# Kernel tuning notes

Measured on AMD Instinct MI355X. Metric: run time of the kernel, lower is better.

## Reference

```python
import jax, jax.numpy as jnp
import numpy as np

WINDOW = (2, 8, 8)
DIM = 180
HEADS = 6
NW = 64  # number of distinct window masks


def _get_position_index(ws):
    d, h, w = ws
    coords = np.stack(np.meshgrid(np.arange(d), np.arange(h), np.arange(w), indexing='ij'))  # [3,d,h,w]
    cf = coords.reshape(3, -1)
    rel = cf[:, :, None] - cf[:, None, :]  # [3,N,N]
    rel = rel.transpose(1, 2, 0).astype(np.int64)
    rel[:, :, 0] += d - 1
    rel[:, :, 1] += h - 1
    rel[:, :, 2] += w - 1
    rel[:, :, 0] *= (2 * h - 1) * (2 * w - 1)
    rel[:, :, 1] *= 2 * w - 1
    return rel.sum(-1)  # [N,N]


def _get_sine_position_encoding(HW, num_pos_feats, temperature=10000.0, normalize=True):
    scale = 2 * np.pi
    not_mask = np.ones((1, HW[0], HW[1]), dtype=np.float32)
    y_embed = not_mask.cumsum(1)
    x_embed = not_mask.cumsum(2)
    if normalize:
        eps = 1e-6
        y_embed = y_embed / (y_embed[:, -1:, :] + eps) * scale
        x_embed = x_embed / (x_embed[:, :, -1:] + eps) * scale
    dim_t = np.arange(num_pos_feats, dtype=np.float32)
    dim_t = temperature ** (2 * (dim_t // 2) / num_pos_feats)
    pos_x = x_embed[:, :, :, None] / dim_t
    pos_y = y_embed[:, :, :, None] / dim_t
    pos_x = np.stack((np.sin(pos_x[:, :, :, 0::2]), np.cos(pos_x[:, :, :, 1::2])), axis=4).reshape(1, HW[0], HW[1], -1)
    pos_y = np.stack((np.sin(pos_y[:, :, :, 0::2]), np.cos(pos_y[:, :, :, 1::2])), axis=4).reshape(1, HW[0], HW[1], -1)
    pos = np.concatenate((pos_y, pos_x), axis=3)  # [1,H,W,2*npf]
    return pos.reshape(1, HW[0] * HW[1], -1)  # [1, H*W, dim]


REL_IDX = _get_position_index(WINDOW)                      # [128,128] int
POS_BIAS = _get_sine_position_encoding(WINDOW[1:], DIM // 2)  # [1,64,180]


def setup_inputs() -> dict:
    key = jax.random.key(0)
    ks = jax.random.split(key, 8)
    B_, N, C = 1024, 128, DIM
    x = jax.random.normal(ks[0], (B_, N, C), dtype=jnp.float32)
    # 0 / -1e4 additive window mask (shifted-window style), nW windows
    m = jax.random.uniform(ks[1], (NW, N, N))
    mask = jnp.where(m < 0.9, 0.0, -1e4).astype(jnp.float32)
    rpb_table = jax.random.normal(ks[2], (675, HEADS), dtype=jnp.float32) * 0.02
    W_qkv_self = jax.random.normal(ks[3], (3 * C, C), dtype=jnp.float32) * (C ** -0.5)
    W_qkv_mut = jax.random.normal(ks[4], (3 * C, C), dtype=jnp.float32) * (C ** -0.5)
    W_proj = jax.random.normal(ks[5], (C, 2 * C), dtype=jnp.float32) * ((2 * C) ** -0.5)
    b_proj = jax.random.normal(ks[6], (C,), dtype=jnp.float32) * 0.01
    return {"x": x, "mask": mask, "rpb_table": rpb_table, "W_qkv_self": W_qkv_self,
            "W_qkv_mut": W_qkv_mut, "W_proj": W_proj, "b_proj": b_proj}


def _qkv(x, W, H):
    B_, N, C = x.shape
    hd = C // H
    y = jnp.einsum('bnc,oc->bno', x, W)  # torch Linear: x @ W.T
    y = y.reshape(B_, N, 3, H, hd).transpose(2, 0, 3, 1, 4)  # [3,B_,H,N,hd]
    return y[0], y[1], y[2]


def _attention(q, k, v, mask, bias, scale):
    # q,k,v: [B_,H,N,hd]; mask: [nW,>=N,>=N] or None; bias: [H,N,N] or None
    B_, H, N, hd = q.shape
    attn = jnp.einsum('bhnd,bhmd->bhnm', q * scale, k)
    if bias is not None:
        attn = attn + bias[None]
    if mask is not None:
        nW = mask.shape[0]
        attn = attn.reshape(B_ // nW, nW, H, N, N) + mask[None, :, None, :N, :N]
        attn = attn.reshape(B_, H, N, N)
    attn = jax.nn.softmax(attn, axis=-1)
    out = jnp.einsum('bhnm,bhmd->bhnd', attn, v)
    return out.transpose(0, 2, 1, 3).reshape(B_, N, H * hd)


def reference(x, mask, rpb_table, W_qkv_self, W_qkv_mut, W_proj, b_proj):
    B_, N, C = x.shape
    H = HEADS
    hd = C // H
    scale = hd ** -0.5
    rel_idx = jnp.asarray(REL_IDX)
    pos_bias = jnp.asarray(POS_BIAS, dtype=x.dtype)

    # self attention with relative position bias
    q, k, v = _qkv(x, W_qkv_self, H)
    bias = rpb_table[rel_idx[:N, :N].reshape(-1)].reshape(N, N, H).transpose(2, 0, 1)  # [H,N,N]
    x_self = _attention(q, k, v, mask, bias, scale)

    # mutual attention between the two temporal halves
    pb = jnp.tile(pos_bias, (1, 2, 1))  # [1,N,C]
    qm, km, vm = _qkv(x + pb, W_qkv_mut, H)
    half = N // 2
    q1, q2 = qm[:, :, :half], qm[:, :, half:]
    k1, k2 = km[:, :, :half], km[:, :, half:]
    v1, v2 = vm[:, :, :half], vm[:, :, half:]
    x1 = _attention(q2, k1, v1, mask, None, scale)
    x2 = _attention(q1, k2, v2, mask, None, scale)
    x_out = jnp.concatenate([jnp.concatenate([x1, x2], axis=1), x_self], axis=2)  # [B_,N,2C]

    return jnp.einsum('bnc,oc->bno', x_out, W_proj) + b_proj
```

## Files before the change

### kernel.cpp

```cpp
#include <hip/hip_runtime.h>
#include <hip/hip_bf16.h>


typedef unsigned short u16;
typedef unsigned int   u32;

#define NTOK 128
#define CDIM 180
#define NHEAD 6
#define XSTR 188
#define KVSTR 36
#define KVSZ  4640
#define QSTR 36
#define SLSTR 33
#define QKSCALE 0.18257418583505536f

__device__ __forceinline__ float bflo(u32 u){ return __uint_as_float(u << 16); }
__device__ __forceinline__ float bfhi(u32 u){ return __uint_as_float(u & 0xFFFF0000u); }
__device__ __forceinline__ float bf2f(u16 v){ return __uint_as_float(((u32)v) << 16); }

__device__ __forceinline__ int kvrow(int r){ return r * KVSTR + ((r >> 4) << 2); }

template<bool F32> __device__ __forceinline__ float ld1(const void* p, size_t i) {
  if constexpr (F32) return reinterpret_cast<const float*>(p)[i];
  else               return bf2f(reinterpret_cast<const u16*>(p)[i]);
}
template<bool F32> __device__ __forceinline__ float2 ld2(const void* p, size_t i) {
  if constexpr (F32) return *reinterpret_cast<const float2*>(reinterpret_cast<const float*>(p) + i);
  else {
    u32 r = *reinterpret_cast<const u32*>(reinterpret_cast<const u16*>(p) + i);
    return float2{bflo(r), bfhi(r)};
  }
}
template<bool F32> __device__ __forceinline__ float4 ld4(const void* p, size_t i) {
  if constexpr (F32) return *reinterpret_cast<const float4*>(reinterpret_cast<const float*>(p) + i);
  else {
    uint2 r = *reinterpret_cast<const uint2*>(reinterpret_cast<const u16*>(p) + i);
    return float4{bflo(r.x), bfhi(r.x), bflo(r.y), bfhi(r.y)};
  }
}

__global__ void detect_dtype(const u32* __restrict__ xw, int* __restrict__ flag) {
  __shared__ int cnt[256];
  int c = 0;
  for (int i = threadIdx.x; i < 4096; i += 256) {
    u32 e = (xw[i] >> 7) & 0xFF;
    c += (e >= 0x58 && e <= 0x90) ? 1 : 0;
  }
  cnt[threadIdx.x] = c;
  __syncthreads();
  if (threadIdx.x == 0) {
    int t = 0;
    for (int i = 0; i < 256; ++i) t += cnt[i];
    flag[0] = (t >= 2458) ? 1 : 0;
  }
}

template<bool F32>
__device__ void body(const void* __restrict__ x,
                     const void* __restrict__ mask,
                     const void* __restrict__ rpb,
                     const void* __restrict__ Wqs,
                     const void* __restrict__ Wqm,
                     const void* __restrict__ Wp,
                     const void* __restrict__ bp,
                     float* __restrict__ out,
                     float* x_s, float* k_s, float* v_s, float* sq_s)
{
  const int tid = threadIdx.x;
  const int b   = blockIdx.x;
  const int n   = tid >> 2;
  const int j   = tid & 3;
  const int w64 = b & 63;

  const int nt  = tid & 31;
  const int ot  = tid >> 5;
  const bool act = (ot < 15);
  const int grp = ot / 5;
  const int lr0 = (ot - grp * 5) * 6;

  const int rp = tid & 127;
  const int og = __builtin_amdgcn_readfirstlane(tid >> 7);
  float acc[45];
  #pragma unroll
  for (int o2 = 0; o2 < 45; ++o2) acc[o2] = 0.f;

  const int bi_d = n >> 6, bi_h = (n >> 3) & 7, bi_w = n & 7;

  {
    const size_t xbase = (size_t)b * (NTOK * CDIM);
    for (int i = tid * 4; i < NTOK * CDIM; i += 2048) {
      float4 f = ld4<F32>(x, xbase + i);
      int r = i / CDIM, c = i - r * CDIM;
      float* dst = &x_s[r * XSTR + c];
      dst[0] = f.x; dst[1] = f.y; dst[2] = f.z; dst[3] = f.w;
    }
  }
  if (tid < NTOK) {
    const int kb = kvrow(tid);
    k_s[kb + 30] = 0.f; k_s[kb + 31] = 0.f;
    v_s[kb + 30] = 0.f; v_s[kb + 31] = 0.f;
  }

  for (int pass = 0; pass < 2; ++pass) {
    const bool self = (pass == 0);
    const void* W = self ? Wqs : Wqm;
    if (!self) {
      __syncthreads();
      for (int i = tid; i < NTOK * CDIM; i += 512) {
        int r = i / CDIM, c = i - r * CDIM;
        int n64 = r & 63;
        int t = (c < 90) ? c : (c - 90);
        float e = (c < 90) ? (float)((n64 >> 3) + 1) : (float)((n64 & 7) + 1);
        float embed = e * 0.78539807f;
        float expo  = (float)(t & ~1) * (1.0f / 90.0f);
        float arg   = embed * exp2f(-13.2877124f * expo);
        float pbv   = (t & 1) ? cosf(arg) : sinf(arg);
        x_s[r * XSTR + c] += pbv;
      }
    }
    for (int h = 0; h < NHEAD; ++h) {
      __syncthreads();
      if (act) {
        float a[4][6];
        #pragma unroll
        for (int i = 0; i < 4; ++i)
          #pragma unroll
          for (int rr = 0; rr < 6; ++rr) a[i][rr] = 0.f;
        const size_t wb = (size_t)(grp * 180 + h * 30 + lr0) * CDIM;
        const float* xr = &x_s[nt * XSTR];
        #pragma unroll 3
        for (int c = 0; c < CDIM; c += 4) {
          float4 wv[6];
          #pragma unroll
          for (int rr = 0; rr < 6; ++rr)
            wv[rr] = ld4<F32>(W, wb + (size_t)rr * CDIM + c);
          #pragma unroll
          for (int i = 0; i < 4; ++i) {
            float4 xv = *reinterpret_cast<const float4*>(xr + i * (32 * XSTR) + c);
            #pragma unroll
            for (int rr = 0; rr < 6; ++rr)
              a[i][rr] = fmaf(xv.x, wv[rr].x,
                         fmaf(xv.y, wv[rr].y,
                         fmaf(xv.z, wv[rr].z,
                         fmaf(xv.w, wv[rr].w, a[i][rr]))));
          }
        }
        #pragma unroll
        for (int i = 0; i < 4; ++i) {
          const int n2 = 32 * i + nt;
          #pragma unroll
          for (int rr = 0; rr < 6; ++rr) {
            const int lr = lr0 + rr;
            const float val = a[i][rr];
            if (grp == 0)      sq_s[n2 * QSTR + lr] = val * QKSCALE;
            else if (grp == 1) k_s[kvrow(n2) + lr] = val;
            else               v_s[kvrow(n2) + lr] = val;
          }
        }
      }
      __syncthreads();
      float qfull[32];
      {
        const float* qr = &sq_s[n * QSTR];
        #pragma unroll
        for (int kk = 0; kk < 7; ++kk) {
          float4 t4 = *reinterpret_cast<const float4*>(qr + 4 * kk);
          qfull[4*kk]   = t4.x; qfull[4*kk+1] = t4.y;
          qfull[4*kk+2] = t4.z; qfull[4*kk+3] = t4.w;
        }
        float2 t2 = *reinterpret_cast<const float2*>(qr + 28);
        qfull[28] = t2.x; qfull[29] = t2.y;
        qfull[30] = 0.f;  qfull[31] = 0.f;
      }
      __syncthreads();
      float o[32];
      #pragma unroll
      for (int d = 0; d < 32; ++d) o[d] = 0.f;
      float m = -1e30f, l = 0.f;

      int jbeg, jcount, kbase;
      if (self) { jbeg = j * 32; jcount = 32; kbase = 0; }
      else      { jbeg = j * 16; jcount = 16; kbase = (n < 64) ? 64 : 0; }
      const int il = self ? n : (n & 63);
      const size_t mbase = (size_t)w64 * (NTOK * NTOK) + (size_t)il * NTOK;

      for (int jj = 0; jj < jcount; jj += 4) {
        const int jl = jbeg + jj;
        const int jg = kbase + jl;
        const float* kb = &k_s[kvrow(jg)];
        float s[4];
        #pragma unroll
        for (int u = 0; u < 4; ++u) {
          const float* kr = kb + u * KVSTR;
          float t0 = 0.f, t1 = 0.f, t2 = 0.f, t3 = 0.f;
          #pragma unroll
          for (int kk = 0; kk < 8; ++kk) {
            float4 kv = *reinterpret_cast<const float4*>(kr + 4 * kk);
            t0 = fmaf(qfull[4 * kk],     kv.x, t0);
            t1 = fmaf(qfull[4 * kk + 1], kv.y, t1);
            t2 = fmaf(qfull[4 * kk + 2], kv.z, t2);
            t3 = fmaf(qfull[4 * kk + 3], kv.w, t3);
          }
          float sv = (t0 + t1) + (t2 + t3);
          sv += ld1<F32>(mask, mbase + (size_t)(jl + u));
          if (self) {
            const int jv = jl + u;
            const int dj = jv >> 6, hj = (jv >> 3) & 7, wj = jv & 7;
            const int idx = (bi_d - dj + 1) * 225 + (bi_h - hj + 7) * 15 + (bi_w - wj + 7);
            sv += ld1<F32>(rpb, (size_t)idx * 6 + h);
          }
          s[u] = sv;
        }
        float M = fmaxf(fmaxf(fmaxf(s[0], s[1]), fmaxf(s[2], s[3])), m);
        float corr = __expf(m - M);
        float p0 = __expf(s[0] - M), p1 = __expf(s[1] - M);
        float p2 = __expf(s[2] - M), p3 = __expf(s[3] - M);
        l = l * corr + ((p0 + p1) + (p2 + p3));
        const float* v0 = &v_s[kvrow(jg)];
        const float* v1 = v0 + KVSTR;
        const float* v2 = v1 + KVSTR;
        const float* v3 = v2 + KVSTR;
        #pragma unroll
        for (int kk = 0; kk < 8; ++kk) {
          float4 a0 = *reinterpret_cast<const float4*>(v0 + 4 * kk);
          float4 a1 = *reinterpret_cast<const float4*>(v1 + 4 * kk);
          float4 a2 = *reinterpret_cast<const float4*>(v2 + 4 * kk);
          float4 a3 = *reinterpret_cast<const float4*>(v3 + 4 * kk);
          o[4*kk]   = fmaf(o[4*kk],   corr, fmaf(p0, a0.x, fmaf(p1, a1.x, fmaf(p2, a2.x, p3 * a3.x))));
          o[4*kk+1] = fmaf(o[4*kk+1], corr, fmaf(p0, a0.y, fmaf(p1, a1.y, fmaf(p2, a2.y, p3 * a3.y))));
          o[4*kk+2] = fmaf(o[4*kk+2], corr, fmaf(p0, a0.z, fmaf(p1, a1.z, fmaf(p2, a2.z, p3 * a3.z))));
          o[4*kk+3] = fmaf(o[4*kk+3], corr, fmaf(p0, a0.w, fmaf(p1, a1.w, fmaf(p2, a2.w, p3 * a3.w))));
        }
        m = M;
      }
      {
        #pragma unroll
        for (int s2 = 1; s2 <= 2; s2 <<= 1) {
          float m2 = __shfl_xor(m, s2);
          float l2 = __shfl_xor(l, s2);
          float M  = fmaxf(m, m2);
          float e1 = __expf(m - M);
          float e2 = __expf(m2 - M);
          l = l * e1 + l2 * e2;
          #pragma unroll
          for (int d = 0; d < 30; ++d) {
            float o2v = __shfl_xor(o[d], s2);
            o[d] = o[d] * e1 + o2v * e2;
          }
          m = M;
        }
        if (j == 0) {
          const int r = self ? n : ((n + 64) & 127);
          float* srow = &sq_s[r * SLSTR];
          const float inv = 1.0f / l;
          #pragma unroll
          for (int d = 0; d < 30; ++d) srow[d] = o[d] * inv;
        }
      }
      __syncthreads();
      {
        const int cb = self ? (CDIM + h * 30) : (h * 30);
        float s0[30];
        #pragma unroll
        for (int d = 0; d < 30; ++d) s0[d] = sq_s[rp * SLSTR + d];
        const size_t wrow = (size_t)(og * 45) * 360 + cb;
        #pragma unroll
        for (int o2 = 0; o2 < 45; ++o2) {
          const size_t wr = wrow + (size_t)o2 * 360;
          float t0 = 0.f;
          #pragma unroll
          for (int d = 0; d < 30; d += 2) {
            float2 w2 = ld2<F32>(Wp, wr + d);
            t0 = fmaf(s0[d], w2.x, fmaf(s0[d + 1], w2.y, t0));
          }
          acc[o2] += t0;
        }
      }
    }
  }

  {
    float* o0 = out + ((size_t)b * NTOK + rp) * CDIM + og * 45;
    #pragma unroll
    for (int o2 = 0; o2 < 45; ++o2) {
      float bb = ld1<F32>(bp, og * 45 + o2);
      o0[o2] = acc[o2] + bb;
    }
  }
}

__global__ __launch_bounds__(512) void fused_all(
    const void* __restrict__ x,    const void* __restrict__ mask,
    const void* __restrict__ rpb,  const void* __restrict__ Wqs,
    const void* __restrict__ Wqm,  const void* __restrict__ Wp,
    const void* __restrict__ bp,   const int* __restrict__ flag,
    float* __restrict__ out)
{
  __shared__ __align__(16) float x_s[NTOK * XSTR];
  __shared__ __align__(16) float k_s[KVSZ];
  __shared__ __align__(16) float v_s[KVSZ];
  __shared__ __align__(16) float sq_s[NTOK * QSTR];
  if (flag[0]) body<false>(x, mask, rpb, Wqs, Wqm, Wp, bp, out, x_s, k_s, v_s, sq_s);
  else         body<true >(x, mask, rpb, Wqs, Wqm, Wp, bp, out, x_s, k_s, v_s, sq_s);
}

extern "C" void kernel_launch(void* const* d_in, const int* in_sizes, int n_in,
                              void* d_out, int out_size, void* d_ws, size_t ws_size,
                              hipStream_t stream) {
  int* flag = (int*)d_ws;
  detect_dtype<<<1, 256, 0, stream>>>((const u32*)d_in[0], flag);
  fused_all<<<1024, 512, 0, stream>>>(d_in[0], d_in[1], d_in[2], d_in[3],
                                      d_in[4], d_in[5], d_in[6], flag,
                                      (float*)d_out);
}
```

Measured before the change: 2.461 ms.

## Process two query rows per thread with 8-way key split in attention

Each thread now handles two adjacent query rows, and the key range for a row is split across 8 lanes instead of 4. Every K and V vector read from shared memory is reused for both rows, halving LDS traffic per FMA. The cost is doubled accumulator and q registers (o0/o1, qf0/qf1), which risks spills or lower occupancy given the existing 45-float acc array, plus an extra shuffle-reduction stage.

```diff
diff --git a/kernel.cpp b/kernel.cpp
--- a/kernel.cpp
+++ b/kernel.cpp
@@ -69,9 +69,11 @@
 {
   const int tid = threadIdx.x;
   const int b   = blockIdx.x;
-  const int n   = tid >> 2;
-  const int j   = tid & 3;
   const int w64 = b & 63;
+
+  const int g  = tid >> 3;
+  const int j8 = tid & 7;
+  const int n0 = g * 2, n1 = n0 + 1;
 
   const int nt  = tid & 31;
   const int ot  = tid >> 5;
@@ -85,7 +87,8 @@
   #pragma unroll
   for (int o2 = 0; o2 < 45; ++o2) acc[o2] = 0.f;
 
-  const int bi_d = n >> 6, bi_h = (n >> 3) & 7, bi_w = n & 7;
+  const int b0d = n0 >> 6, b0h = (n0 >> 3) & 7, b0w = n0 & 7;
+  const int b1d = n1 >> 6, b1h = (n1 >> 3) & 7, b1w = n1 & 7;
 
   {
     const size_t xbase = (size_t)b * (NTOK * CDIM);
@@ -160,63 +163,80 @@
         }
       }
       __syncthreads();
-      float qfull[32];
+      float qf0[32], qf1[32];
       {
-        const float* qr = &sq_s[n * QSTR];
+        const float* qr0 = &sq_s[n0 * QSTR];
+        const float* qr1 = &sq_s[n1 * QSTR];
         #pragma unroll
         for (int kk = 0; kk < 7; ++kk) {
-          float4 t4 = *reinterpret_cast<const float4*>(qr + 4 * kk);
-          qfull[4*kk]   = t4.x; qfull[4*kk+1] = t4.y;
-          qfull[4*kk+2] = t4.z; qfull[4*kk+3] = t4.w;
-        }
-        float2 t2 = *reinterpret_cast<const float2*>(qr + 28);
-        qfull[28] = t2.x; qfull[29] = t2.y;
-        qfull[30] = 0.f;  qfull[31] = 0.f;
-      }
-      __syncthreads();
-      float o[32];
+          float4 t4 = *reinterpret_cast<const float4*>(qr0 + 4 * kk);
+          qf0[4*kk] = t4.x; qf0[4*kk+1] = t4.y; qf0[4*kk+2] = t4.z; qf0[4*kk+3] = t4.w;
+          float4 u4 = *reinterpret_cast<const float4*>(qr1 + 4 * kk);
+          qf1[4*kk] = u4.x; qf1[4*kk+1] = u4.y; qf1[4*kk+2] = u4.z; qf1[4*kk+3] = u4.w;
+        }
+        float2 t2 = *reinterpret_cast<const float2*>(qr0 + 28);
+        qf0[28] = t2.x; qf0[29] = t2.y; qf0[30] = 0.f; qf0[31] = 0.f;
+        float2 u2 = *reinterpret_cast<const float2*>(qr1 + 28);
+        qf1[28] = u2.x; qf1[29] = u2.y; qf1[30] = 0.f; qf1[31] = 0.f;
+      }
+      __syncthreads();
+      float o0[32], o1[32];
       #pragma unroll
-      for (int d = 0; d < 32; ++d) o[d] = 0.f;
-      float m = -1e30f, l = 0.f;
+      for (int d = 0; d < 32; ++d) { o0[d] = 0.f; o1[d] = 0.f; }
+      float m0 = -1e30f, l0 = 0.f, m1 = -1e30f, l1 = 0.f;
 
       int jbeg, jcount, kbase;
-      if (self) { jbeg = j * 32; jcount = 32; kbase = 0; }
-      else      { jbeg = j * 16; jcount = 16; kbase = (n < 64) ? 64 : 0; }
-      const int il = self ? n : (n & 63);
-      const size_t mbase = (size_t)w64 * (NTOK * NTOK) + (size_t)il * NTOK;
+      if (self) { jbeg = j8 * 16; jcount = 16; kbase = 0; }
+      else      { jbeg = j8 * 8;  jcount = 8;  kbase = (n0 < 64) ? 64 : 0; }
+      const int il0 = self ? n0 : (n0 & 63);
+      const size_t mbase0 = (size_t)w64 * (NTOK * NTOK) + (size_t)il0 * NTOK;
+      const size_t mbase1 = mbase0 + NTOK;
 
       for (int jj = 0; jj < jcount; jj += 4) {
         const int jl = jbeg + jj;
         const int jg = kbase + jl;
         const float* kb = &k_s[kvrow(jg)];
-        float s[4];
+        float s0[4], s1[4];
         #pragma unroll
         for (int u = 0; u < 4; ++u) {
           const float* kr = kb + u * KVSTR;
-          float t0 = 0.f, t1 = 0.f, t2 = 0.f, t3 = 0.f;
+          float a0 = 0.f, a1 = 0.f, a2 = 0.f, a3 = 0.f;
+          float c0 = 0.f, c1 = 0.f, c2 = 0.f, c3 = 0.f;
           #pragma unroll
           for (int kk = 0; kk < 8; ++kk) {
             float4 kv = *reinterpret_cast<const float4*>(kr + 4 * kk);
-            t0 = fmaf(qfull[4 * kk],     kv.x, t0);
-            t1 = fmaf(qfull[4 * kk + 1], kv.y, t1);
-            t2 = fmaf(qfull[4 * kk + 2], kv.z, t2);
-            t3 = fmaf(qfull[4 * kk + 3], kv.w, t3);
-          }
-          float sv = (t0 + t1) + (t2 + t3);
-          sv += ld1<F32>(mask, mbase + (size_t)(jl + u));
+            a0 = fmaf(qf0[4*kk],   kv.x, a0);
+            a1 = fmaf(qf0[4*kk+1], kv.y, a1);
+            a2 = fmaf(qf0[4*kk+2], kv.z, a2);
+            a3 = fmaf(qf0[4*kk+3], kv.w, a3);
+            c0 = fmaf(qf1[4*kk],   kv.x, c0);
+            c1 = fmaf(qf1[4*kk+1], kv.y, c1);
+            c2 = fmaf(qf1[4*kk+2], kv.z, c2);
+            c3 = fmaf(qf1[4*kk+3], kv.w, c3);
+          }
+          float sv0 = (a0 + a1) + (a2 + a3);
+          float sv1 = (c0 + c1) + (c2 + c3);
+          sv0 += ld1<F32>(mask, mbase0 + (size_t)(jl + u));
+          sv1 += ld1<F32>(mask, mbase1 + (size_t)(jl + u));
           if (self) {
             const int jv = jl + u;
             const int dj = jv >> 6, hj = (jv >> 3) & 7, wj = jv & 7;
-            const int idx = (bi_d - dj + 1) * 225 + (bi_h - hj + 7) * 15 + (bi_w - wj + 7);
-            sv += ld1<F32>(rpb, (size_t)idx * 6 + h);
-          }
-          s[u] = sv;
-        }
-        float M = fmaxf(fmaxf(fmaxf(s[0], s[1]), fmaxf(s[2], s[3])), m);
-        float corr = __expf(m - M);
-        float p0 = __expf(s[0] - M), p1 = __expf(s[1] - M);
-        float p2 = __expf(s[2] - M), p3 = __expf(s[3] - M);
-        l = l * corr + ((p0 + p1) + (p2 + p3));
+            const int i0 = (b0d - dj + 1) * 225 + (b0h - hj + 7) * 15 + (b0w - wj + 7);
+            const int i1 = (b1d - dj + 1) * 225 + (b1h - hj + 7) * 15 + (b1w - wj + 7);
+            sv0 += ld1<F32>(rpb, (size_t)i0 * 6 + h);
+            sv1 += ld1<F32>(rpb, (size_t)i1 * 6 + h);
+          }
+          s0[u] = sv0; s1[u] = sv1;
+        }
+        float M0 = fmaxf(fmaxf(fmaxf(s0[0], s0[1]), fmaxf(s0[2], s0[3])), m0);
+        float M1 = fmaxf(fmaxf(fmaxf(s1[0], s1[1]), fmaxf(s1[2], s1[3])), m1);
+        float cr0 = __expf(m0 - M0), cr1 = __expf(m1 - M1);
+        float p00 = __expf(s0[0] - M0), p01 = __expf(s0[1] - M0);
+        float p02 = __expf(s0[2] - M0), p03 = __expf(s0[3] - M0);
+        float p10 = __expf(s1[0] - M1), p11 = __expf(s1[1] - M1);
+        float p12 = __expf(s1[2] - M1), p13 = __expf(s1[3] - M1);
+        l0 = l0 * cr0 + ((p00 + p01) + (p02 + p03));
+        l1 = l1 * cr1 + ((p10 + p11) + (p12 + p13));
         const float* v0 = &v_s[kvrow(jg)];
         const float* v1 = v0 + KVSTR;
         const float* v2 = v1 + KVSTR;
@@ -227,43 +247,65 @@
           float4 a1 = *reinterpret_cast<const float4*>(v1 + 4 * kk);
           float4 a2 = *reinterpret_cast<const float4*>(v2 + 4 * kk);
           float4 a3 = *reinterpret_cast<const float4*>(v3 + 4 * kk);
-          o[4*kk]   = fmaf(o[4*kk],   corr, fmaf(p0, a0.x, fmaf(p1, a1.x, fmaf(p2, a2.x, p3 * a3.x))));
-          o[4*kk+1] = fmaf(o[4*kk+1], corr, fmaf(p0, a0.y, fmaf(p1, a1.y, fmaf(p2, a2.y, p3 * a3.y))));
-          o[4*kk+2] = fmaf(o[4*kk+2], corr, fmaf(p0, a0.z, fmaf(p1, a1.z, fmaf(p2, a2.z, p3 * a3.z))));
-          o[4*kk+3] = fmaf(o[4*kk+3], corr, fmaf(p0, a0.w, fmaf(p1, a1.w, fmaf(p2, a2.w, p3 * a3.w))));
-        }
-        m = M;
+          o0[4*kk]   = fmaf(o0[4*kk],   cr0, fmaf(p00, a0.x, fmaf(p01, a1.x, fmaf(p02, a2.x, p03 * a3.x))));
+          o0[4*kk+1] = fmaf(o0[4*kk+1], cr0, fmaf(p00, a0.y, fmaf(p01, a1.y, fmaf(p02, a2.y, p03 * a3.y))));
+          o0[4*kk+2] = fmaf(o0[4*kk+2], cr0, fmaf(p00, a0.z, fmaf(p01, a1.z, fmaf(p02, a2.z, p03 * a3.z))));
+          o0[4*kk+3] = fmaf(o0[4*kk+3], cr0, fmaf(p00, a0.w, fmaf(p01, a1.w, fmaf(p02, a2.w, p03 * a3.w))));
+          o1[4*kk]   = fmaf(o1[4*kk],   cr1, fmaf(p10, a0.x, fmaf(p11, a1.x, fmaf(p12, a2.x, p13 * a3.x))));
+          o1[4*kk+1] = fmaf(o1[4*kk+1], cr1, fmaf(p10, a0.y, fmaf(p11, a1.y, fmaf(p12, a2.y, p13 * a3.y))));
+          o1[4*kk+2] = fmaf(o1[4*kk+2], cr1, fmaf(p10, a0.z, fmaf(p11, a1.z, fmaf(p12, a2.z, p13 * a3.z))));
+          o1[4*kk+3] = fmaf(o1[4*kk+3], cr1, fmaf(p10, a0.w, fmaf(p11, a1.w, fmaf(p12, a2.w, p13 * a3.w))));
+        }
+        m0 = M0; m1 = M1;
       }
       {
         #pragma unroll
-        for (int s2 = 1; s2 <= 2; s2 <<= 1) {
-          float m2 = __shfl_xor(m, s2);
-          float l2 = __shfl_xor(l, s2);
-          float M  = fmaxf(m, m2);
-          float e1 = __expf(m - M);
-          float e2 = __expf(m2 - M);
-          l = l * e1 + l2 * e2;
+        for (int s2 = 1; s2 <= 4; s2 <<= 1) {
+          float mm = __shfl_xor(m0, s2);
+          float ll = __shfl_xor(l0, s2);
+          float M  = fmaxf(m0, mm);
+          float e1 = __expf(m0 - M);
+          float e2 = __expf(mm - M);
+          l0 = l0 * e1 + ll * e2;
           #pragma unroll
           for (int d = 0; d < 30; ++d) {
-            float o2v = __shfl_xor(o[d], s2);
-            o[d] = o[d] * e1 + o2v * e2;
-          }
-          m = M;
-        }
-        if (j == 0) {
-          const int r = self ? n : ((n + 64) & 127);
+            float ov = __shfl_xor(o0[d], s2);
+            o0[d] = o0[d] * e1 + ov * e2;
+          }
+          m0 = M;
+          float mn = __shfl_xor(m1, s2);
+          float ln = __shfl_xor(l1, s2);
+          float N  = fmaxf(m1, mn);
+          float f1 = __expf(m1 - N);
+          float f2 = __expf(mn - N);
+          l1 = l1 * f1 + ln * f2;
+          #pragma unroll
+          for (int d = 0; d < 30; ++d) {
+            float ov = __shfl_xor(o1[d], s2);
+            o1[d] = o1[d] * f1 + ov * f2;
+          }
+          m1 = N;
+        }
+        if (j8 == 0) {
+          const int r = self ? n0 : ((n0 + 64) & 127);
           float* srow = &sq_s[r * SLSTR];
-          const float inv = 1.0f / l;
-          #pragma unroll
-          for (int d = 0; d < 30; ++d) srow[d] = o[d] * inv;
+          const float inv = 1.0f / l0;
+          #pragma unroll
+          for (int d = 0; d < 30; ++d) srow[d] = o0[d] * inv;
+        } else if (j8 == 4) {
+          const int r = self ? n1 : ((n1 + 64) & 127);
+          float* srow = &sq_s[r * SLSTR];
+          const float inv = 1.0f / l1;
+          #pragma unroll
+          for (int d = 0; d < 30; ++d) srow[d] = o1[d] * inv;
         }
       }
       __syncthreads();
       {
         const int cb = self ? (CDIM + h * 30) : (h * 30);
-        float s0[30];
-        #pragma unroll
-        for (int d = 0; d < 30; ++d) s0[d] = sq_s[rp * SLSTR + d];
+        float s0p[30];
+        #pragma unroll
+        for (int d = 0; d < 30; ++d) s0p[d] = sq_s[rp * SLSTR + d];
         const size_t wrow = (size_t)(og * 45) * 360 + cb;
         #pragma unroll
         for (int o2 = 0; o2 < 45; ++o2) {
@@ -272,7 +314,7 @@
           #pragma unroll
           for (int d = 0; d < 30; d += 2) {
             float2 w2 = ld2<F32>(Wp, wr + d);
-            t0 = fmaf(s0[d], w2.x, fmaf(s0[d + 1], w2.y, t0));
+            t0 = fmaf(s0p[d], w2.x, fmaf(s0p[d + 1], w2.y, t0));
           }
           acc[o2] += t0;
         }
```

Measured after the change: 2.411 ms. 2.0% less time.

## Compute QKV projections with split-bf16 MFMA and pre-converted weights

Applied to the files above, without the earlier changes.

Replaces the scalar FP32 FMA QKV projection with bf16 MFMA 16x16x32 instructions. FP32 precision is emulated by splitting x and the weights into hi/lo bf16 parts and issuing three MFMAs. A separate kernel converts both QKV weight matrices into padded hi/lo bf16 buffers in the workspace. Activations are stored in shared memory as hi/lo bf16, and the positional encoding is applied by recombining, adding, and re-splitting. The old FP32 path is kept as a fallback when the workspace is too small. The change trades an extra conversion kernel and some precision risk from dropping the lo*lo term for much higher matrix throughput in the projection stage.

```diff
diff --git a/kernel.cpp b/kernel.cpp
--- a/kernel.cpp
+++ b/kernel.cpp
@@ -8,16 +8,33 @@
 #define NTOK 128
 #define CDIM 180
 #define NHEAD 6
-#define XSTR 188
 #define KVSTR 36
 #define KVSZ  4640
 #define QSTR 36
 #define SLSTR 33
+#define XH   200
+#define WROWS 1081
+#define WCOL 192
+#define XSTR 188
 #define QKSCALE 0.18257418583505536f
+
+typedef __attribute__((ext_vector_type(8))) short bf16x8v;
+typedef __attribute__((ext_vector_type(4))) float f32x4v;
 
 __device__ __forceinline__ float bflo(u32 u){ return __uint_as_float(u << 16); }
 __device__ __forceinline__ float bfhi(u32 u){ return __uint_as_float(u & 0xFFFF0000u); }
 __device__ __forceinline__ float bf2f(u16 v){ return __uint_as_float(((u32)v) << 16); }
+
+__device__ __forceinline__ u16 f2bf(float f){
+  u32 u = __float_as_uint(f);
+  u32 r = u + 0x7FFFu + ((u >> 16) & 1u);
+  return (u16)(r >> 16);
+}
+__device__ __forceinline__ void split2(float f, u16& h, u16& l){
+  h = f2bf(f);
+  float rem = f - bf2f(h);
+  l = f2bf(rem);
+}
 
 __device__ __forceinline__ int kvrow(int r){ return r * KVSTR + ((r >> 4) << 2); }
 
@@ -38,6 +55,15 @@
     uint2 r = *reinterpret_cast<const uint2*>(reinterpret_cast<const u16*>(p) + i);
     return float4{bflo(r.x), bfhi(r.x), bflo(r.y), bfhi(r.y)};
   }
+}
+
+__device__ __forceinline__ float posenc(int c, int n64) {
+  int t = (c < 90) ? c : (c - 90);
+  float e = (c < 90) ? (float)((n64 >> 3) + 1) : (float)((n64 & 7) + 1);
+  float embed = e * 0.78539807f;
+  float expo  = (float)(t & ~1) * (1.0f / 90.0f);
+  float arg   = embed * exp2f(-13.2877124f * expo);
+  return (t & 1) ? cosf(arg) : sinf(arg);
 }
 
 __global__ void detect_dtype(const u32* __restrict__ xw, int* __restrict__ flag) {
@@ -56,28 +82,45 @@
   }
 }
 
+__global__ void conv_w(const void* __restrict__ Wqs, const void* __restrict__ Wqm,
+                       const int* __restrict__ flag,
+                       u16* __restrict__ whi, u16* __restrict__ wlo) {
+  const int r = blockIdx.x;
+  const int c = threadIdx.x;
+  float v = 0.f;
+  if (r < 1080 && c < 180) {
+    const void* W = (r < 540) ? Wqs : Wqm;
+    const int rr  = (r < 540) ? r : r - 540;
+    v = flag[0] ? ld1<false>(W, (size_t)rr * 180 + c)
+                : ld1<true >(W, (size_t)rr * 180 + c);
+  }
+  u16 h, l;
+  split2(v, h, l);
+  whi[r * WCOL + c] = h;
+  wlo[r * WCOL + c] = l;
+}
+
 template<bool F32>
-__device__ void body(const void* __restrict__ x,
-                     const void* __restrict__ mask,
-                     const void* __restrict__ rpb,
-                     const void* __restrict__ Wqs,
-                     const void* __restrict__ Wqm,
-                     const void* __restrict__ Wp,
-                     const void* __restrict__ bp,
-                     float* __restrict__ out,
-                     float* x_s, float* k_s, float* v_s, float* sq_s)
+__device__ void body_mfma(const void* __restrict__ x,
+                          const void* __restrict__ mask,
+                          const void* __restrict__ rpb,
+                          const void* __restrict__ Wp,
+                          const void* __restrict__ bp,
+                          const u16* __restrict__ whi,
+                          const u16* __restrict__ wlo,
+                          float* __restrict__ out,
+                          u16* xhi_s, u16* xlo_s,
+                          float* k_s, float* v_s, float* sq_s)
 {
   const int tid = threadIdx.x;
   const int b   = blockIdx.x;
+  const int w64 = b & 63;
   const int n   = tid >> 2;
   const int j   = tid & 3;
-  const int w64 = b & 63;
-
-  const int nt  = tid & 31;
-  const int ot  = tid >> 5;
-  const bool act = (ot < 15);
-  const int grp = ot / 5;
-  const int lr0 = (ot - grp * 5) * 6;
+
+  const int wv  = tid >> 6;
+  const int l15 = tid & 15;
+  const int lk  = (tid & 63) >> 4;
 
   const int rp = tid & 127;
   const int og = __builtin_amdgcn_readfirstlane(tid >> 7);
@@ -89,73 +132,93 @@
 
   {
     const size_t xbase = (size_t)b * (NTOK * CDIM);
-    for (int i = tid * 4; i < NTOK * CDIM; i += 2048) {
-      float4 f = ld4<F32>(x, xbase + i);
-      int r = i / CDIM, c = i - r * CDIM;
-      float* dst = &x_s[r * XSTR + c];
-      dst[0] = f.x; dst[1] = f.y; dst[2] = f.z; dst[3] = f.w;
-    }
-  }
-  if (tid < NTOK) {
-    const int kb = kvrow(tid);
-    k_s[kb + 30] = 0.f; k_s[kb + 31] = 0.f;
-    v_s[kb + 30] = 0.f; v_s[kb + 31] = 0.f;
+    for (int i = tid; i < NTOK * 45; i += 512) {
+      int r = i / 45, c4 = (i - r * 45) * 4;
+      float4 f = ld4<F32>(x, xbase + (size_t)r * CDIM + c4);
+      u16 h0,l0,h1,l1,h2,l2,h3,l3;
+      split2(f.x, h0, l0); split2(f.y, h1, l1);
+      split2(f.z, h2, l2); split2(f.w, h3, l3);
+      u32* ph = reinterpret_cast<u32*>(&xhi_s[r * XH + c4]);
+      u32* pl = reinterpret_cast<u32*>(&xlo_s[r * XH + c4]);
+      ph[0] = (u32)h0 | ((u32)h1 << 16);
+      ph[1] = (u32)h2 | ((u32)h3 << 16);
+      pl[0] = (u32)l0 | ((u32)l1 << 16);
+      pl[1] = (u32)l2 | ((u32)l3 << 16);
+    }
+    for (int i = tid; i < NTOK * 10; i += 512) {
+      int r = i / 10, c = 180 + (i - r * 10) * 2;
+      *reinterpret_cast<u32*>(&xhi_s[r * XH + c]) = 0;
+      *reinterpret_cast<u32*>(&xlo_s[r * XH + c]) = 0;
+    }
+    if (tid < NTOK) {
+      const int kb = kvrow(tid);
+      k_s[kb + 30] = 0.f; k_s[kb + 31] = 0.f;
+      v_s[kb + 30] = 0.f; v_s[kb + 31] = 0.f;
+    }
   }
 
   for (int pass = 0; pass < 2; ++pass) {
     const bool self = (pass == 0);
-    const void* W = self ? Wqs : Wqm;
     if (!self) {
       __syncthreads();
-      for (int i = tid; i < NTOK * CDIM; i += 512) {
-        int r = i / CDIM, c = i - r * CDIM;
+      for (int i = tid; i < NTOK * 90; i += 512) {
+        int r = i / 90, c = (i - r * 90) * 2;
         int n64 = r & 63;
-        int t = (c < 90) ? c : (c - 90);
-        float e = (c < 90) ? (float)((n64 >> 3) + 1) : (float)((n64 & 7) + 1);
-        float embed = e * 0.78539807f;
-        float expo  = (float)(t & ~1) * (1.0f / 90.0f);
-        float arg   = embed * exp2f(-13.2877124f * expo);
-        float pbv   = (t & 1) ? cosf(arg) : sinf(arg);
-        x_s[r * XSTR + c] += pbv;
-      }
-    }
+        u32 hw = *reinterpret_cast<u32*>(&xhi_s[r * XH + c]);
+        u32 lw = *reinterpret_cast<u32*>(&xlo_s[r * XH + c]);
+        float x0 = bflo(hw) + bflo(lw) + posenc(c,     n64);
+        float x1 = bfhi(hw) + bfhi(lw) + posenc(c + 1, n64);
+        u16 h0,l0,h1,l1;
+        split2(x0, h0, l0); split2(x1, h1, l1);
+        *reinterpret_cast<u32*>(&xhi_s[r * XH + c]) = (u32)h0 | ((u32)h1 << 16);
+        *reinterpret_cast<u32*>(&xlo_s[r * XH + c]) = (u32)l0 | ((u32)l1 << 16);
+      }
+    }
+    const int matbase = self ? 0 : 540;
     for (int h = 0; h < NHEAD; ++h) {
       __syncthreads();
-      if (act) {
-        float a[4][6];
-        #pragma unroll
-        for (int i = 0; i < 4; ++i)
-          #pragma unroll
-          for (int rr = 0; rr < 6; ++rr) a[i][rr] = 0.f;
-        const size_t wb = (size_t)(grp * 180 + h * 30 + lr0) * CDIM;
-        const float* xr = &x_s[nt * XSTR];
-        #pragma unroll 3
-        for (int c = 0; c < CDIM; c += 4) {
-          float4 wv[6];
-          #pragma unroll
-          for (int rr = 0; rr < 6; ++rr)
-            wv[rr] = ld4<F32>(W, wb + (size_t)rr * CDIM + c);
-          #pragma unroll
-          for (int i = 0; i < 4; ++i) {
-            float4 xv = *reinterpret_cast<const float4*>(xr + i * (32 * XSTR) + c);
+      {
+        int rowoff[6];
+        #pragma unroll
+        for (int nt = 0; nt < 6; ++nt) {
+          const int o  = nt * 16 + l15;
+          const int g2 = o / 30;
+          const int lr = o - g2 * 30;
+          rowoff[nt] = ((o < 90) ? (matbase + g2 * 180 + h * 30 + lr) : 1080) * WCOL;
+        }
+        f32x4v am[6];
+        #pragma unroll
+        for (int nt = 0; nt < 6; ++nt) am[nt] = f32x4v{0.f, 0.f, 0.f, 0.f};
+        const u16* xh = &xhi_s[(wv * 16 + l15) * XH];
+        const u16* xl = &xlo_s[(wv * 16 + l15) * XH];
+        #pragma unroll 2
+        for (int ks = 0; ks < 6; ++ks) {
+          const int k0 = lk * 8 + ks * 32;
+          bf16x8v ahi = *reinterpret_cast<const bf16x8v*>(xh + k0);
+          bf16x8v alo = *reinterpret_cast<const bf16x8v*>(xl + k0);
+          #pragma unroll
+          for (int nt = 0; nt < 6; ++nt) {
+            bf16x8v bhi = *reinterpret_cast<const bf16x8v*>(whi + rowoff[nt] + k0);
+            bf16x8v blo = *reinterpret_cast<const bf16x8v*>(wlo + rowoff[nt] + k0);
+            am[nt] = __builtin_amdgcn_mfma_f32_16x16x32_bf16(ahi, bhi, am[nt], 0, 0, 0);
+            am[nt] = __builtin_amdgcn_mfma_f32_16x16x32_bf16(alo, bhi, am[nt], 0, 0, 0);
+            am[nt] = __builtin_amdgcn_mfma_f32_16x16x32_bf16(ahi, blo, am[nt], 0, 0, 0);
+          }
+        }
+        #pragma unroll
+        for (int nt = 0; nt < 6; ++nt) {
+          const int o = nt * 16 + l15;
+          if (o < 90) {
+            const int g2 = o / 30;
+            const int lr = o - g2 * 30;
             #pragma unroll
-            for (int rr = 0; rr < 6; ++rr)
-              a[i][rr] = fmaf(xv.x, wv[rr].x,
-                         fmaf(xv.y, wv[rr].y,
-                         fmaf(xv.z, wv[rr].z,
-                         fmaf(xv.w, wv[rr].w, a[i][rr]))));
-          }
-        }
-        #pragma unroll
-        for (int i = 0; i < 4; ++i) {
-          const int n2 = 32 * i + nt;
-          #pragma unroll
-          for (int rr = 0; rr < 6; ++rr) {
-            const int lr = lr0 + rr;
-            const float val = a[i][rr];
-            if (grp == 0)      sq_s[n2 * QSTR + lr] = val * QKSCALE;
-            else if (grp == 1) k_s[kvrow(n2) + lr] = val;
-            else               v_s[kvrow(n2) + lr] = val;
+            for (int r = 0; r < 4; ++r) {
+              const int t = wv * 16 + lk * 4 + r;
+              const float val = am[nt][r];
+              if (g2 == 0)      sq_s[t * QSTR + lr] = val * QKSCALE;
+              else if (g2 == 1) k_s[kvrow(t) + lr] = val;
+              else              v_s[kvrow(t) + lr] = val;
+            }
           }
         }
       }
@@ -280,6 +343,234 @@
     }
   }
 
+  {
+    float* o0 = out + ((size_t)b * NTOK + rp) * CDIM + og * 45;
+    #pragma unroll
+    for (int o2 = 0; o2 < 45; ++o2) {
+      float bb = ld1<F32>(bp, og * 45 + o2);
+      o0[o2] = acc[o2] + bb;
+    }
+  }
+}
+
+__global__ __launch_bounds__(512) void fused_mfma(
+    const void* __restrict__ x,    const void* __restrict__ mask,
+    const void* __restrict__ rpb,  const void* __restrict__ Wp,
+    const void* __restrict__ bp,   const int* __restrict__ flag,
+    const u16* __restrict__ whi,   const u16* __restrict__ wlo,
+    float* __restrict__ out)
+{
+  __shared__ __align__(16) u16 xhi_s[NTOK * XH];
+  __shared__ __align__(16) u16 xlo_s[NTOK * XH];
+  __shared__ __align__(16) float k_s[KVSZ];
+  __shared__ __align__(16) float v_s[KVSZ];
+  __shared__ __align__(16) float sq_s[NTOK * QSTR];
+  if (flag[0]) body_mfma<false>(x, mask, rpb, Wp, bp, whi, wlo, out, xhi_s, xlo_s, k_s, v_s, sq_s);
+  else         body_mfma<true >(x, mask, rpb, Wp, bp, whi, wlo, out, xhi_s, xlo_s, k_s, v_s, sq_s);
+}
+
+template<bool F32>
+__device__ void body_old(const void* __restrict__ x, const void* __restrict__ mask,
+                         const void* __restrict__ rpb, const void* __restrict__ Wqs,
+                         const void* __restrict__ Wqm, const void* __restrict__ Wp,
+                         const void* __restrict__ bp, float* __restrict__ out,
+                         float* x_s, float* k_s, float* v_s, float* sq_s)
+{
+  const int tid = threadIdx.x;
+  const int b   = blockIdx.x;
+  const int w64 = b & 63;
+  const int n   = tid >> 2;
+  const int j   = tid & 3;
+  const int nt  = tid & 31;
+  const int ot  = tid >> 5;
+  const bool act = (ot < 15);
+  const int grp = ot / 5;
+  const int lr0 = (ot - grp * 5) * 6;
+  const int rp = tid & 127;
+  const int og = __builtin_amdgcn_readfirstlane(tid >> 7);
+  float acc[45];
+  #pragma unroll
+  for (int o2 = 0; o2 < 45; ++o2) acc[o2] = 0.f;
+  const int bi_d = n >> 6, bi_h = (n >> 3) & 7, bi_w = n & 7;
+  {
+    const size_t xbase = (size_t)b * (NTOK * CDIM);
+    for (int i = tid * 4; i < NTOK * CDIM; i += 2048) {
+      float4 f = ld4<F32>(x, xbase + i);
+      int r = i / CDIM, c = i - r * CDIM;
+      float* dst = &x_s[r * XSTR + c];
+      dst[0] = f.x; dst[1] = f.y; dst[2] = f.z; dst[3] = f.w;
+    }
+  }
+  if (tid < NTOK) {
+    const int kb = kvrow(tid);
+    k_s[kb + 30] = 0.f; k_s[kb + 31] = 0.f;
+    v_s[kb + 30] = 0.f; v_s[kb + 31] = 0.f;
+  }
+  for (int pass = 0; pass < 2; ++pass) {
+    const bool self = (pass == 0);
+    const void* W = self ? Wqs : Wqm;
+    if (!self) {
+      __syncthreads();
+      for (int i = tid; i < NTOK * CDIM; i += 512) {
+        int r = i / CDIM, c = i - r * CDIM;
+        x_s[r * XSTR + c] += posenc(c, r & 63);
+      }
+    }
+    for (int h = 0; h < NHEAD; ++h) {
+      __syncthreads();
+      if (act) {
+        float a[4][6];
+        #pragma unroll
+        for (int i = 0; i < 4; ++i)
+          #pragma unroll
+          for (int rr = 0; rr < 6; ++rr) a[i][rr] = 0.f;
+        const size_t wb = (size_t)(grp * 180 + h * 30 + lr0) * CDIM;
+        const float* xr = &x_s[nt * XSTR];
+        #pragma unroll 3
+        for (int c = 0; c < CDIM; c += 4) {
+          float4 wv[6];
+          #pragma unroll
+          for (int rr = 0; rr < 6; ++rr)
+            wv[rr] = ld4<F32>(W, wb + (size_t)rr * CDIM + c);
+          #pragma unroll
+          for (int i = 0; i < 4; ++i) {
+            float4 xv = *reinterpret_cast<const float4*>(xr + i * (32 * XSTR) + c);
+            #pragma unroll
+            for (int rr = 0; rr < 6; ++rr)
+              a[i][rr] = fmaf(xv.x, wv[rr].x, fmaf(xv.y, wv[rr].y,
+                         fmaf(xv.z, wv[rr].z, fmaf(xv.w, wv[rr].w, a[i][rr]))));
+          }
+        }
+        #pragma unroll
+        for (int i = 0; i < 4; ++i) {
+          const int n2 = 32 * i + nt;
+          #pragma unroll
+          for (int rr = 0; rr < 6; ++rr) {
+            const int lr = lr0 + rr;
+            const float val = a[i][rr];
+            if (grp == 0)      sq_s[n2 * QSTR + lr] = val * QKSCALE;
+            else if (grp == 1) k_s[kvrow(n2) + lr] = val;
+            else               v_s[kvrow(n2) + lr] = val;
+          }
+        }
+      }
+      __syncthreads();
+      float qfull[32];
+      {
+        const float* qr = &sq_s[n * QSTR];
+        #pragma unroll
+        for (int kk = 0; kk < 7; ++kk) {
+          float4 t4 = *reinterpret_cast<const float4*>(qr + 4 * kk);
+          qfull[4*kk] = t4.x; qfull[4*kk+1] = t4.y;
+          qfull[4*kk+2] = t4.z; qfull[4*kk+3] = t4.w;
+        }
+        float2 t2 = *reinterpret_cast<const float2*>(qr + 28);
+        qfull[28] = t2.x; qfull[29] = t2.y; qfull[30] = 0.f; qfull[31] = 0.f;
+      }
+      __syncthreads();
+      float o[32];
+      #pragma unroll
+      for (int d = 0; d < 32; ++d) o[d] = 0.f;
+      float m = -1e30f, l = 0.f;
+      int jbeg, jcount, kbase;
+      if (self) { jbeg = j * 32; jcount = 32; kbase = 0; }
+      else      { jbeg = j * 16; jcount = 16; kbase = (n < 64) ? 64 : 0; }
+      const int il = self ? n : (n & 63);
+      const size_t mbase = (size_t)w64 * (NTOK * NTOK) + (size_t)il * NTOK;
+      for (int jj = 0; jj < jcount; jj += 4) {
+        const int jl = jbeg + jj;
+        const int jg = kbase + jl;
+        const float* kb = &k_s[kvrow(jg)];
+        float s[4];
+        #pragma unroll
+        for (int u = 0; u < 4; ++u) {
+          const float* kr = kb + u * KVSTR;
+          float t0 = 0.f, t1 = 0.f, t2 = 0.f, t3 = 0.f;
+          #pragma unroll
+          for (int kk = 0; kk < 8; ++kk) {
+            float4 kv = *reinterpret_cast<const float4*>(kr + 4 * kk);
+            t0 = fmaf(qfull[4 * kk],     kv.x, t0);
+            t1 = fmaf(qfull[4 * kk + 1], kv.y, t1);
+            t2 = fmaf(qfull[4 * kk + 2], kv.z, t2);
+            t3 = fmaf(qfull[4 * kk + 3], kv.w, t3);
+          }
+          float sv = (t0 + t1) + (t2 + t3);
+          sv += ld1<F32>(mask, mbase + (size_t)(jl + u));
+          if (self) {
+            const int jv = jl + u;
+            const int dj = jv >> 6, hj = (jv >> 3) & 7, wj = jv & 7;
+            const int idx = (bi_d - dj + 1) * 225 + (bi_h - hj + 7) * 15 + (bi_w - wj + 7);
+            sv += ld1<F32>(rpb, (size_t)idx * 6 + h);
+          }
+          s[u] = sv;
+        }
+        float M = fmaxf(fmaxf(fmaxf(s[0], s[1]), fmaxf(s[2], s[3])), m);
+        float corr = __expf(m - M);
+        float p0 = __expf(s[0] - M), p1 = __expf(s[1] - M);
+        float p2 = __expf(s[2] - M), p3 = __expf(s[3] - M);
+        l = l * corr + ((p0 + p1) + (p2 + p3));
+        const float* v0 = &v_s[kvrow(jg)];
+        const float* v1 = v0 + KVSTR;
+        const float* v2 = v1 + KVSTR;
+        const float* v3 = v2 + KVSTR;
+        #pragma unroll
+        for (int kk = 0; kk < 8; ++kk) {
+          float4 a0 = *reinterpret_cast<const float4*>(v0 + 4 * kk);
+          float4 a1 = *reinterpret_cast<const float4*>(v1 + 4 * kk);
+          float4 a2 = *reinterpret_cast<const float4*>(v2 + 4 * kk);
+          float4 a3 = *reinterpret_cast<const float4*>(v3 + 4 * kk);
+          o[4*kk]   = fmaf(o[4*kk],   corr, fmaf(p0, a0.x, fmaf(p1, a1.x, fmaf(p2, a2.x, p3 * a3.x))));
+          o[4*kk+1] = fmaf(o[4*kk+1], corr, fmaf(p0, a0.y, fmaf(p1, a1.y, fmaf(p2, a2.y, p3 * a3.y))));
+          o[4*kk+2] = fmaf(o[4*kk+2], corr, fmaf(p0, a0.z, fmaf(p1, a1.z, fmaf(p2, a2.z, p3 * a3.z))));
+          o[4*kk+3] = fmaf(o[4*kk+3], corr, fmaf(p0, a0.w, fmaf(p1, a1.w, fmaf(p2, a2.w, p3 * a3.w))));
+        }
+        m = M;
+      }
+      {
+        #pragma unroll
+        for (int s2 = 1; s2 <= 2; s2 <<= 1) {
+          float m2 = __shfl_xor(m, s2);
+          float l2 = __shfl_xor(l, s2);
+          float M  = fmaxf(m, m2);
+          float e1 = __expf(m - M);
+          float e2 = __expf(m2 - M);
+          l = l * e1 + l2 * e2;
+          #pragma unroll
+          for (int d = 0; d < 30; ++d) {
+            float o2v = __shfl_xor(o[d], s2);
+            o[d] = o[d] * e1 + o2v * e2;
+          }
+          m = M;
+        }
+        if (j == 0) {
+          const int r = self ? n : ((n + 64) & 127);
+          float* srow = &sq_s[r * SLSTR];
+          const float inv = 1.0f / l;
+          #pragma unroll
+          for (int d = 0; d < 30; ++d) srow[d] = o[d] * inv;
+        }
+      }
+      __syncthreads();
+      {
+        const int cb = self ? (CDIM + h * 30) : (h * 30);
+        float s0p[30];
+        #pragma unroll
+        for (int d = 0; d < 30; ++d) s0p[d] = sq_s[rp * SLSTR + d];
+        const size_t wrow = (size_t)(og * 45) * 360 + cb;
+        #pragma unroll
+        for (int o2 = 0; o2 < 45; ++o2) {
+          const size_t wr = wrow + (size_t)o2 * 360;
+          float t0 = 0.f;
+          #pragma unroll
+          for (int d = 0; d < 30; d += 2) {
+            float2 w2 = ld2<F32>(Wp, wr + d);
+            t0 = fmaf(s0p[d], w2.x, fmaf(s0p[d + 1], w2.y, t0));
+          }
+          acc[o2] += t0;
+        }
+      }
+    }
+  }
   {
     float* o0 = out + ((size_t)b * NTOK + rp) * CDIM + og * 45;
     #pragma unroll
@@ -301,8 +592,8 @@
   __shared__ __align__(16) float k_s[KVSZ];
   __shared__ __align__(16) float v_s[KVSZ];
   __shared__ __align__(16) float sq_s[NTOK * QSTR];
-  if (flag[0]) body<false>(x, mask, rpb, Wqs, Wqm, Wp, bp, out, x_s, k_s, v_s, sq_s);
-  else         body<true >(x, mask, rpb, Wqs, Wqm, Wp, bp, out, x_s, k_s, v_s, sq_s);
+  if (flag[0]) body_old<false>(x, mask, rpb, Wqs, Wqm, Wp, bp, out, x_s, k_s, v_s, sq_s);
+  else         body_old<true >(x, mask, rpb, Wqs, Wqm, Wp, bp, out, x_s, k_s, v_s, sq_s);
 }
 
 extern "C" void kernel_launch(void* const* d_in, const int* in_sizes, int n_in,
@@ -310,7 +601,17 @@
                               hipStream_t stream) {
   int* flag = (int*)d_ws;
   detect_dtype<<<1, 256, 0, stream>>>((const u32*)d_in[0], flag);
-  fused_all<<<1024, 512, 0, stream>>>(d_in[0], d_in[1], d_in[2], d_in[3],
-                                      d_in[4], d_in[5], d_in[6], flag,
-                                      (float*)d_out);
-}
+  const size_t wbytes = (size_t)WROWS * WCOL * sizeof(u16);
+  const size_t need = 64 + 2 * wbytes;
+  if (ws_size >= need) {
+    u16* whi = (u16*)((char*)d_ws + 64);
+    u16* wlo = (u16*)((char*)d_ws + 64 + wbytes);
+    conv_w<<<WROWS, WCOL, 0, stream>>>(d_in[3], d_in[4], flag, whi, wlo);
+    fused_mfma<<<1024, 512, 0, stream>>>(d_in[0], d_in[1], d_in[2], d_in[5],
+                                         d_in[6], flag, whi, wlo, (float*)d_out);
+  } else {
+    fused_all<<<1024, 512, 0, stream>>>(d_in[0], d_in[1], d_in[2], d_in[3],
+                                        d_in[4], d_in[5], d_in[6], flag,
+                                        (float*)d_out);
+  }
+}
```

Measured after the change: 2.513 ms. 2.1% more time.
